# Kernel tuning notes

Measured on AMD Instinct MI355X. Metric: run time of the kernel, lower is better.

The kernel has to match this reference:

```python
import jax, jax.numpy as jnp
import numpy as np

DIM = 1024
FF = 4096
BATCH = 4
SEQ = 2048
EPS = 1e-5


def setup_inputs() -> dict:
    key = jax.random.key(0)
    ks = jax.random.split(key, 8)
    x = jax.random.normal(ks[0], (BATCH, SEQ, DIM), dtype=jnp.float32)
    # phazor init: exp(2j*pi*arange(dim)/dim) * |randn(dim)|
    ang = 2.0 * np.pi * jnp.arange(DIM, dtype=jnp.float32) / DIM
    mag = jnp.abs(jax.random.normal(ks[1], (DIM,), dtype=jnp.float32))
    phazor_re = mag * jnp.cos(ang)
    phazor_im = mag * jnp.sin(ang)
    last_re = jax.random.normal(ks[2], (DIM,), dtype=jnp.float32)
    last_im = jax.random.normal(ks[3], (DIM,), dtype=jnp.float32)
    w1 = jax.random.normal(ks[4], (FF, DIM), dtype=jnp.float32) * DIM ** -0.5
    b1 = jnp.zeros((FF,), dtype=jnp.float32)
    w2 = jax.random.normal(ks[5], (DIM, FF), dtype=jnp.float32) * FF ** -0.5
    b2 = jnp.zeros((DIM,), dtype=jnp.float32)
    return {
        'x': x,
        'ln1_w': jnp.ones((DIM,), jnp.float32), 'ln1_b': jnp.zeros((DIM,), jnp.float32),
        'ln2_w': jnp.ones((DIM,), jnp.float32), 'ln2_b': jnp.zeros((DIM,), jnp.float32),
        'sc_lin': jnp.ones((DIM,), jnp.float32),
        'phazor_re': phazor_re, 'phazor_im': phazor_im,
        'last_re': last_re, 'last_im': last_im,
        'w1': w1, 'b1': b1, 'w2': w2, 'b2': b2,
    }


def _layer_norm(x, w, b):
    mu = jnp.mean(x, axis=-1, keepdims=True)
    var = jnp.mean(jnp.square(x - mu), axis=-1, keepdims=True)
    return (x - mu) * jax.lax.rsqrt(var + EPS) * w + b


def _sconv(x, phazor_re, phazor_im, last_re, last_im):
    B, L, D = x.shape
    dtype = x.dtype
    xc = x.astype(jnp.complex64)
    p_raw = phazor_re + 1j * phazor_im
    # tanh(|p|) * exp(i*angle(p))
    p = (jnp.tanh(jnp.abs(p_raw)) * jnp.exp(1j * jnp.angle(p_raw))).astype(jnp.complex64)
    t = jnp.arange(L)[:, None]
    prog = jnp.power(p[None, :], t)            # [L, D] complex
    filt_fft = jnp.fft.fft(prog, n=2 * L, axis=0)   # [2L, D]
    x_fft = jnp.fft.fft(xc, n=2 * L, axis=1)        # [B, 2L, D]
    conv = jnp.fft.ifft(filt_fft[None] * x_fft, axis=1)[:, :L]  # [B, L, D]
    last = (last_re + 1j * last_im)[None, None, :]  # [1,1,D] broadcast over batch
    conv_with_past = conv + last * prog[None] * p[None, None]
    return conv_with_past.real.astype(dtype)


def reference(x, ln1_w, ln1_b, ln2_w, ln2_b, sc_lin,
              phazor_re, phazor_im, last_re, last_im,
              w1, b1, w2, b2):
    # SConv branch
    x_res = x
    h = _layer_norm(x, ln1_w, ln1_b)
    h = jax.nn.silu(h)
    h = _sconv(h, phazor_re, phazor_im, last_re, last_im)
    h = h * sc_lin
    x = h + x_res
    # FFN branch
    x_res = x
    h = _layer_norm(x, ln2_w, ln2_b)
    h = jax.nn.silu(jnp.einsum('bld,fd->blf', h, w1) + b1)
    h = jnp.einsum('blf,df->bld', h, w2) + b2
    return h + x_res
```

## Files before the change

kernel.cpp:

```cpp
#include <hip/hip_runtime.h>
#include <cmath>


#define DIMD 1024
#define FFD  4096
#define BATCH 4
#define SEQL 2048
#define MROWS (BATCH*SEQL)
#define EPSF 1e-5f
#define CHUNKS 32
#define CLEN (SEQL/CHUNKS)

typedef __attribute__((ext_vector_type(8))) _Float16 half8;
typedef __attribute__((ext_vector_type(4))) _Float16 half4;
typedef __attribute__((ext_vector_type(4))) float    floatx4;

#define H_OFF    0u
#define E_OFF    33554432u
#define SIN_OFF  34603008u
#define H2_OFF   35651584u
#define W1H_OFF  52428800u
#define W2H_OFF  60817408u
#define Y1_OFF   69206016u

__device__ __forceinline__ void load_lds16(const _Float16* g, _Float16* l) {
    __builtin_amdgcn_global_load_lds(
        (const __attribute__((address_space(1))) unsigned int*)g,
        (__attribute__((address_space(3))) unsigned int*)l,
        16, 0, 0);
}

__global__ __launch_bounds__(256)
void cast_f32_f16(const float* __restrict__ src, _Float16* __restrict__ dst) {
    int i = (blockIdx.x * 256 + threadIdx.x) * 4;
    float4 v = *(const float4*)(src + i);
    half4 o;
    o.x = (_Float16)v.x; o.y = (_Float16)v.y; o.z = (_Float16)v.z; o.w = (_Float16)v.w;
    *(half4*)(dst + i) = o;
}

__global__ __launch_bounds__(256)
void ln_kernel(const float* __restrict__ x, const float* __restrict__ w,
               const float* __restrict__ b, float* __restrict__ of,
               _Float16* __restrict__ oh, int mode) {
    const size_t row = blockIdx.x;
    const int tid = threadIdx.x;
    float4 v = *(const float4*)(x + row * DIMD + tid * 4);
    float s = (v.x + v.y) + (v.z + v.w);
    float q = (v.x * v.x + v.y * v.y) + (v.z * v.z + v.w * v.w);
    #pragma unroll
    for (int off = 32; off; off >>= 1) {
        s += __shfl_down(s, off, 64);
        q += __shfl_down(q, off, 64);
    }
    __shared__ float red[8];
    if (!(tid & 63)) { red[tid >> 6] = s; red[4 + (tid >> 6)] = q; }
    __syncthreads();
    s = (red[0] + red[1]) + (red[2] + red[3]);
    q = (red[4] + red[5]) + (red[6] + red[7]);
    const float mu = s * (1.f / DIMD);
    const float rs = rsqrtf(q * (1.f / DIMD) - mu * mu + EPSF);
    float4 wv = *(const float4*)(w + tid * 4);
    float4 bv = *(const float4*)(b + tid * 4);
    float o0 = (v.x - mu) * rs * wv.x + bv.x;
    float o1 = (v.y - mu) * rs * wv.y + bv.y;
    float o2 = (v.z - mu) * rs * wv.z + bv.z;
    float o3 = (v.w - mu) * rs * wv.w + bv.w;
    if (mode == 1) {
        o0 = o0 / (1.f + __expf(-o0));
        o1 = o1 / (1.f + __expf(-o1));
        o2 = o2 / (1.f + __expf(-o2));
        o3 = o3 / (1.f + __expf(-o3));
        float4 ov = {o0, o1, o2, o3};
        *(float4*)(of + row * DIMD + tid * 4) = ov;
    } else {
        half4 hv;
        hv.x = (_Float16)o0; hv.y = (_Float16)o1;
        hv.z = (_Float16)o2; hv.w = (_Float16)o3;
        *(half4*)(oh + row * DIMD + tid * 4) = hv;
    }
}

__device__ __forceinline__ void get_p(const float* pre, const float* pim, int d,
                                      float& pr, float& pi) {
    float re = pre[d], im = pim[d];
    float r = sqrtf(re * re + im * im);
    float t = tanhf(r) / fmaxf(r, 1e-30f);
    pr = re * t; pi = im * t;
}

__global__ __launch_bounds__(256)
void scan_partial(const float* __restrict__ h, const float* __restrict__ pre,
                  const float* __restrict__ pim, float2* __restrict__ e) {
    const int d = blockIdx.x * 256 + threadIdx.x;
    const int c = blockIdx.y;
    const int bb = blockIdx.z;
    float pr, pi; get_p(pre, pim, d, pr, pi);
    float sr = 0.f, si = 0.f;
    const float* hp = h + ((size_t)bb * SEQL + (size_t)c * CLEN) * DIMD + d;
    #pragma unroll 4
    for (int j = 0; j < CLEN; ++j) {
        float hv = hp[(size_t)j * DIMD];
        float nr = pr * sr - pi * si + hv;
        float ni = pr * si + pi * sr;
        sr = nr; si = ni;
    }
    e[((size_t)bb * CHUNKS + c) * DIMD + d] = make_float2(sr, si);
}

__global__ __launch_bounds__(256)
void scan_combine(const float2* __restrict__ e, const float* __restrict__ pre,
                  const float* __restrict__ pim, const float* __restrict__ lre,
                  const float* __restrict__ lim, float2* __restrict__ sv) {
    const int d = blockIdx.x * 256 + threadIdx.x;
    const int bb = blockIdx.y;
    float pr, pi; get_p(pre, pim, d, pr, pi);
    float qr = pr, qi = pi;
    #pragma unroll
    for (int s = 0; s < 6; ++s) {
        float nr = qr * qr - qi * qi;
        float ni = 2.f * qr * qi;
        qr = nr; qi = ni;
    }
    float sr = lre[d], si = lim[d];
    for (int c = 0; c < CHUNKS; ++c) {
        sv[((size_t)bb * CHUNKS + c) * DIMD + d] = make_float2(sr, si);
        float2 ec = e[((size_t)bb * CHUNKS + c) * DIMD + d];
        float nr = qr * sr - qi * si + ec.x;
        float ni = qr * si + qi * sr + ec.y;
        sr = nr; si = ni;
    }
}

__global__ __launch_bounds__(256)
void scan_final(const float* __restrict__ h, const float* __restrict__ x,
                const float* __restrict__ pre, const float* __restrict__ pim,
                const float* __restrict__ sc, const float2* __restrict__ sv,
                float* __restrict__ x2) {
    const int d = blockIdx.x * 256 + threadIdx.x;
    const int c = blockIdx.y;
    const int bb = blockIdx.z;
    float pr, pi; get_p(pre, pim, d, pr, pi);
    float2 s0 = sv[((size_t)bb * CHUNKS + c) * DIMD + d];
    float sr = s0.x, si = s0.y;
    const float scd = sc[d];
    const size_t base = ((size_t)bb * SEQL + (size_t)c * CLEN) * DIMD + d;
    #pragma unroll 4
    for (int j = 0; j < CLEN; ++j) {
        float hv = h[base + (size_t)j * DIMD];
        float nr = pr * sr - pi * si + hv;
        float ni = pr * si + pi * sr;
        sr = nr; si = ni;
        x2[base + (size_t)j * DIMD] = x[base + (size_t)j * DIMD] + scd * sr;
    }
}

#define BM 128
#define BN 128
#define BK 64

__global__ __launch_bounds__(256)
void gemm_bt(const _Float16* __restrict__ A, const _Float16* __restrict__ W,
             const float* __restrict__ bias, _Float16* __restrict__ out_h,
             const float* resid, float* out_f, int N, int K, int epi) {
    __shared__ _Float16 As[BM * BK];
    __shared__ _Float16 Bs[BN * BK];
    const int tid  = threadIdx.x;
    const int lane = tid & 63;
    const int wave = tid >> 6;
    const int wm = (wave >> 1) * 64;
    const int wn = (wave & 1) * 64;
    const size_t m0 = (size_t)blockIdx.y * BM;
    const size_t n0 = (size_t)blockIdx.x * BN;
    const int fr = lane & 15;
    const int quad = lane >> 4;

    const int srow = wave * 32 + (lane >> 3);
    const int ccp  = ((lane & 7) ^ (lane >> 3)) * 8;
    const _Float16* ag = A + (m0 + srow) * (size_t)K + ccp;
    const _Float16* wg = W + (n0 + srow) * (size_t)K + ccp;
    _Float16* asl = &As[(wave * 32) * BK];
    _Float16* bsl = &Bs[(wave * 32) * BK];

    floatx4 acc[4][4] = {};

    for (int k0 = 0; k0 < K; k0 += BK) {
        #pragma unroll
        for (int t = 0; t < 4; ++t) {
            load_lds16(ag + k0 + (size_t)(t * 8) * K, asl + t * 8 * BK);
            load_lds16(wg + k0 + (size_t)(t * 8) * K, bsl + t * 8 * BK);
        }
        __syncthreads();
        #pragma unroll
        for (int kk = 0; kk < BK; kk += 32) {
            half8 af[4], bf[4];
            #pragma unroll
            for (int i = 0; i < 4; ++i) {
                const int slot = (((kk >> 3) + quad) ^ (fr & 7)) * 8;
                af[i] = *(const half8*)(&As[(wm + i * 16 + fr) * BK + slot]);
                bf[i] = *(const half8*)(&Bs[(wn + i * 16 + fr) * BK + slot]);
            }
            #pragma unroll
            for (int i = 0; i < 4; ++i)
                #pragma unroll
                for (int j = 0; j < 4; ++j)
                    acc[i][j] = __builtin_amdgcn_mfma_f32_16x16x32_f16(
                        af[i], bf[j], acc[i][j], 0, 0, 0);
        }
        __syncthreads();
    }

    #pragma unroll
    for (int i = 0; i < 4; ++i) {
        #pragma unroll
        for (int j = 0; j < 4; ++j) {
            #pragma unroll
            for (int r = 0; r < 4; ++r) {
                const size_t gm = m0 + wm + i * 16 + quad * 4 + r;
                const size_t gn = n0 + wn + j * 16 + fr;
                float v = acc[i][j][r] + bias[gn];
                if (epi == 1) {
                    float sl = v / (1.f + __expf(-v));
                    out_h[gm * N + gn] = (_Float16)sl;
                } else {
                    out_f[gm * N + gn] = v + resid[gm * N + gn];
                }
            }
        }
    }
}

extern "C" void kernel_launch(void* const* d_in, const int* in_sizes, int n_in,
                              void* d_out, int out_size, void* d_ws, size_t ws_size,
                              hipStream_t stream) {
    const float* x    = (const float*)d_in[0];
    const float* ln1w = (const float*)d_in[1];
    const float* ln1b = (const float*)d_in[2];
    const float* ln2w = (const float*)d_in[3];
    const float* ln2b = (const float*)d_in[4];
    const float* sc   = (const float*)d_in[5];
    const float* pre  = (const float*)d_in[6];
    const float* pim  = (const float*)d_in[7];
    const float* lre  = (const float*)d_in[8];
    const float* lim  = (const float*)d_in[9];
    const float* w1   = (const float*)d_in[10];
    const float* b1   = (const float*)d_in[11];
    const float* w2   = (const float*)d_in[12];
    const float* b2   = (const float*)d_in[13];

    char* ws = (char*)d_ws;
    float*      h   = (float*)(ws + H_OFF);
    float2*     e   = (float2*)(ws + E_OFF);
    float2*     sv  = (float2*)(ws + SIN_OFF);
    _Float16*   h2  = (_Float16*)(ws + H2_OFF);
    _Float16*   w1h = (_Float16*)(ws + W1H_OFF);
    _Float16*   w2h = (_Float16*)(ws + W2H_OFF);
    _Float16*   y1  = (_Float16*)(ws + Y1_OFF);
    float*      x2  = (float*)d_out;
    float*      outp = (float*)d_out;

    cast_f32_f16<<<dim3(FFD * DIMD / 1024), 256, 0, stream>>>(w1, w1h);
    cast_f32_f16<<<dim3(FFD * DIMD / 1024), 256, 0, stream>>>(w2, w2h);
    ln_kernel<<<dim3(MROWS), 256, 0, stream>>>(x, ln1w, ln1b, h, nullptr, 1);
    scan_partial<<<dim3(DIMD / 256, CHUNKS, BATCH), 256, 0, stream>>>(h, pre, pim, e);
    scan_combine<<<dim3(DIMD / 256, BATCH), 256, 0, stream>>>(e, pre, pim, lre, lim, sv);
    scan_final<<<dim3(DIMD / 256, CHUNKS, BATCH), 256, 0, stream>>>(h, x, pre, pim, sc, sv, x2);
    ln_kernel<<<dim3(MROWS), 256, 0, stream>>>(x2, ln2w, ln2b, nullptr, h2, 2);
    gemm_bt<<<dim3(FFD / BN, MROWS / BM), 256, 0, stream>>>(
        h2, w1h, b1, y1, nullptr, nullptr, FFD, DIMD, 1);
    gemm_bt<<<dim3(DIMD / BN, MROWS / BM), 256, 0, stream>>>(
        y1, w2h, b2, nullptr, x2, outp, DIMD, FFD, 2);
}
```

Before: 382.4 us.

## Fuse layernorms and SiLU into chunked scan passes, merge weight casts

Each scan pass now owns one (chunk, batch) row block and recomputes LN1 and SiLU on the fly, so the fp32 intermediate h buffer disappears. The second pass also computes LN2 and writes the fp16 GEMM input directly, which removes both standalone layernorm kernels and their global round trips. Chunk count is raised to 128 to keep enough blocks, and the two weight casts are merged into one launch. In exchange, LN1 is recomputed in both passes, each row step needs block-wide barriers, and only 512 blocks run the sequential loops.

```diff
diff --git a/kernel.cpp b/kernel.cpp
--- a/kernel.cpp
+++ b/kernel.cpp
@@ -8,20 +8,19 @@
 #define SEQL 2048
 #define MROWS (BATCH*SEQL)
 #define EPSF 1e-5f
-#define CHUNKS 32
+#define CHUNKS 128
 #define CLEN (SEQL/CHUNKS)
 
 typedef __attribute__((ext_vector_type(8))) _Float16 half8;
 typedef __attribute__((ext_vector_type(4))) _Float16 half4;
 typedef __attribute__((ext_vector_type(4))) float    floatx4;
 
-#define H_OFF    0u
-#define E_OFF    33554432u
-#define SIN_OFF  34603008u
-#define H2_OFF   35651584u
-#define W1H_OFF  52428800u
-#define W2H_OFF  60817408u
-#define Y1_OFF   69206016u
+#define E_OFF    0u
+#define SV_OFF   4194304u
+#define H2_OFF   8388608u
+#define W1H_OFF  25165824u
+#define W2H_OFF  33554432u
+#define Y1_OFF   41943040u
 
 __device__ __forceinline__ void load_lds16(const _Float16* g, _Float16* l) {
     __builtin_amdgcn_global_load_lds(
@@ -30,54 +29,11 @@
         16, 0, 0);
 }
 
-__global__ __launch_bounds__(256)
-void cast_f32_f16(const float* __restrict__ src, _Float16* __restrict__ dst) {
-    int i = (blockIdx.x * 256 + threadIdx.x) * 4;
-    float4 v = *(const float4*)(src + i);
-    half4 o;
-    o.x = (_Float16)v.x; o.y = (_Float16)v.y; o.z = (_Float16)v.z; o.w = (_Float16)v.w;
-    *(half4*)(dst + i) = o;
-}
-
-__global__ __launch_bounds__(256)
-void ln_kernel(const float* __restrict__ x, const float* __restrict__ w,
-               const float* __restrict__ b, float* __restrict__ of,
-               _Float16* __restrict__ oh, int mode) {
-    const size_t row = blockIdx.x;
-    const int tid = threadIdx.x;
-    float4 v = *(const float4*)(x + row * DIMD + tid * 4);
-    float s = (v.x + v.y) + (v.z + v.w);
-    float q = (v.x * v.x + v.y * v.y) + (v.z * v.z + v.w * v.w);
+__device__ __forceinline__ void wave_reduce2(float& s, float& q) {
     #pragma unroll
     for (int off = 32; off; off >>= 1) {
         s += __shfl_down(s, off, 64);
         q += __shfl_down(q, off, 64);
-    }
-    __shared__ float red[8];
-    if (!(tid & 63)) { red[tid >> 6] = s; red[4 + (tid >> 6)] = q; }
-    __syncthreads();
-    s = (red[0] + red[1]) + (red[2] + red[3]);
-    q = (red[4] + red[5]) + (red[6] + red[7]);
-    const float mu = s * (1.f / DIMD);
-    const float rs = rsqrtf(q * (1.f / DIMD) - mu * mu + EPSF);
-    float4 wv = *(const float4*)(w + tid * 4);
-    float4 bv = *(const float4*)(b + tid * 4);
-    float o0 = (v.x - mu) * rs * wv.x + bv.x;
-    float o1 = (v.y - mu) * rs * wv.y + bv.y;
-    float o2 = (v.z - mu) * rs * wv.z + bv.z;
-    float o3 = (v.w - mu) * rs * wv.w + bv.w;
-    if (mode == 1) {
-        o0 = o0 / (1.f + __expf(-o0));
-        o1 = o1 / (1.f + __expf(-o1));
-        o2 = o2 / (1.f + __expf(-o2));
-        o3 = o3 / (1.f + __expf(-o3));
-        float4 ov = {o0, o1, o2, o3};
-        *(float4*)(of + row * DIMD + tid * 4) = ov;
-    } else {
-        half4 hv;
-        hv.x = (_Float16)o0; hv.y = (_Float16)o1;
-        hv.z = (_Float16)o2; hv.w = (_Float16)o3;
-        *(half4*)(oh + row * DIMD + tid * 4) = hv;
     }
 }
 
@@ -90,22 +46,62 @@
 }
 
 __global__ __launch_bounds__(256)
-void scan_partial(const float* __restrict__ h, const float* __restrict__ pre,
-                  const float* __restrict__ pim, float2* __restrict__ e) {
-    const int d = blockIdx.x * 256 + threadIdx.x;
-    const int c = blockIdx.y;
-    const int bb = blockIdx.z;
-    float pr, pi; get_p(pre, pim, d, pr, pi);
-    float sr = 0.f, si = 0.f;
-    const float* hp = h + ((size_t)bb * SEQL + (size_t)c * CLEN) * DIMD + d;
-    #pragma unroll 4
+void cast2_f32_f16(const float* __restrict__ w1, const float* __restrict__ w2,
+                   _Float16* __restrict__ o1, _Float16* __restrict__ o2) {
+    int i = (blockIdx.x * 256 + threadIdx.x) * 4;
+    const float* src = w1;
+    _Float16* dst = o1;
+    if (i >= FFD * DIMD) { i -= FFD * DIMD; src = w2; dst = o2; }
+    float4 v = *(const float4*)(src + i);
+    half4 o;
+    o.x = (_Float16)v.x; o.y = (_Float16)v.y; o.z = (_Float16)v.z; o.w = (_Float16)v.w;
+    *(half4*)(dst + i) = o;
+}
+
+__global__ __launch_bounds__(256)
+void scan_phase1(const float* __restrict__ x, const float* __restrict__ lw,
+                 const float* __restrict__ lb, const float* __restrict__ pre,
+                 const float* __restrict__ pim, float2* __restrict__ e) {
+    const int tid = threadIdx.x;
+    const int d0 = tid * 4;
+    const int c = blockIdx.x, bb = blockIdx.y;
+    const int lane = tid & 63, wave = tid >> 6;
+    __shared__ float2 red[2][4];
+
+    float pr[4], pi[4], sr[4] = {}, si[4] = {};
+    #pragma unroll
+    for (int q = 0; q < 4; ++q) get_p(pre, pim, d0 + q, pr[q], pi[q]);
+    const float4 wv = *(const float4*)(lw + d0);
+    const float4 bv = *(const float4*)(lb + d0);
+    const size_t rowbase = ((size_t)bb * SEQL + (size_t)c * CLEN) * DIMD;
+
     for (int j = 0; j < CLEN; ++j) {
-        float hv = hp[(size_t)j * DIMD];
-        float nr = pr * sr - pi * si + hv;
-        float ni = pr * si + pi * sr;
-        sr = nr; si = ni;
-    }
-    e[((size_t)bb * CHUNKS + c) * DIMD + d] = make_float2(sr, si);
+        float4 v = *(const float4*)(x + rowbase + (size_t)j * DIMD + d0);
+        float s = (v.x + v.y) + (v.z + v.w);
+        float q2 = (v.x * v.x + v.y * v.y) + (v.z * v.z + v.w * v.w);
+        wave_reduce2(s, q2);
+        if (lane == 0) red[j & 1][wave] = make_float2(s, q2);
+        __syncthreads();
+        float2 r0 = red[j & 1][0], r1 = red[j & 1][1];
+        float2 r2 = red[j & 1][2], r3 = red[j & 1][3];
+        s = (r0.x + r1.x) + (r2.x + r3.x);
+        q2 = (r0.y + r1.y) + (r2.y + r3.y);
+        const float mu = s * (1.f / DIMD);
+        const float rs = rsqrtf(q2 * (1.f / DIMD) - mu * mu + EPSF);
+        float o[4] = {
+            (v.x - mu) * rs * wv.x + bv.x, (v.y - mu) * rs * wv.y + bv.y,
+            (v.z - mu) * rs * wv.z + bv.z, (v.w - mu) * rs * wv.w + bv.w };
+        #pragma unroll
+        for (int q = 0; q < 4; ++q) {
+            float hv = o[q] / (1.f + __expf(-o[q]));
+            float nr = pr[q] * sr[q] - pi[q] * si[q] + hv;
+            float ni = pr[q] * si[q] + pi[q] * sr[q];
+            sr[q] = nr; si[q] = ni;
+        }
+    }
+    float2* ep = e + ((size_t)bb * CHUNKS + c) * DIMD + d0;
+    #pragma unroll
+    for (int q = 0; q < 4; ++q) ep[q] = make_float2(sr[q], si[q]);
 }
 
 __global__ __launch_bounds__(256)
@@ -117,15 +113,17 @@
     float pr, pi; get_p(pre, pim, d, pr, pi);
     float qr = pr, qi = pi;
     #pragma unroll
-    for (int s = 0; s < 6; ++s) {
+    for (int s = 0; s < 4; ++s) {
         float nr = qr * qr - qi * qi;
         float ni = 2.f * qr * qi;
         qr = nr; qi = ni;
     }
     float sr = lre[d], si = lim[d];
+    #pragma unroll 4
     for (int c = 0; c < CHUNKS; ++c) {
-        sv[((size_t)bb * CHUNKS + c) * DIMD + d] = make_float2(sr, si);
-        float2 ec = e[((size_t)bb * CHUNKS + c) * DIMD + d];
+        const size_t idx = ((size_t)bb * CHUNKS + c) * DIMD + d;
+        sv[idx] = make_float2(sr, si);
+        float2 ec = e[idx];
         float nr = qr * sr - qi * si + ec.x;
         float ni = qr * si + qi * sr + ec.y;
         sr = nr; si = ni;
@@ -133,25 +131,83 @@
 }
 
 __global__ __launch_bounds__(256)
-void scan_final(const float* __restrict__ h, const float* __restrict__ x,
-                const float* __restrict__ pre, const float* __restrict__ pim,
-                const float* __restrict__ sc, const float2* __restrict__ sv,
-                float* __restrict__ x2) {
-    const int d = blockIdx.x * 256 + threadIdx.x;
-    const int c = blockIdx.y;
-    const int bb = blockIdx.z;
-    float pr, pi; get_p(pre, pim, d, pr, pi);
-    float2 s0 = sv[((size_t)bb * CHUNKS + c) * DIMD + d];
-    float sr = s0.x, si = s0.y;
-    const float scd = sc[d];
-    const size_t base = ((size_t)bb * SEQL + (size_t)c * CLEN) * DIMD + d;
-    #pragma unroll 4
+void scan_phase2(const float* __restrict__ x, const float* __restrict__ l1w,
+                 const float* __restrict__ l1b, const float* __restrict__ l2w,
+                 const float* __restrict__ l2b, const float* __restrict__ pre,
+                 const float* __restrict__ pim, const float* __restrict__ sc,
+                 const float2* __restrict__ sv, float* __restrict__ x2,
+                 _Float16* __restrict__ h2) {
+    const int tid = threadIdx.x;
+    const int d0 = tid * 4;
+    const int c = blockIdx.x, bb = blockIdx.y;
+    const int lane = tid & 63, wave = tid >> 6;
+    __shared__ float2 redA[2][4];
+    __shared__ float2 redB[2][4];
+
+    float pr[4], pi[4], sr[4], si[4];
+    #pragma unroll
+    for (int q = 0; q < 4; ++q) {
+        get_p(pre, pim, d0 + q, pr[q], pi[q]);
+        float2 s0 = sv[((size_t)bb * CHUNKS + c) * DIMD + d0 + q];
+        sr[q] = s0.x; si[q] = s0.y;
+    }
+    const float4 w1v = *(const float4*)(l1w + d0);
+    const float4 b1v = *(const float4*)(l1b + d0);
+    const float4 w2v = *(const float4*)(l2w + d0);
+    const float4 b2v = *(const float4*)(l2b + d0);
+    const float4 scv = *(const float4*)(sc + d0);
+    const size_t rowbase = ((size_t)bb * SEQL + (size_t)c * CLEN) * DIMD;
+
     for (int j = 0; j < CLEN; ++j) {
-        float hv = h[base + (size_t)j * DIMD];
-        float nr = pr * sr - pi * si + hv;
-        float ni = pr * si + pi * sr;
-        sr = nr; si = ni;
-        x2[base + (size_t)j * DIMD] = x[base + (size_t)j * DIMD] + scd * sr;
+        float4 v = *(const float4*)(x + rowbase + (size_t)j * DIMD + d0);
+        float s = (v.x + v.y) + (v.z + v.w);
+        float q2 = (v.x * v.x + v.y * v.y) + (v.z * v.z + v.w * v.w);
+        wave_reduce2(s, q2);
+        if (lane == 0) redA[j & 1][wave] = make_float2(s, q2);
+        __syncthreads();
+        {
+            float2 r0 = redA[j & 1][0], r1 = redA[j & 1][1];
+            float2 r2 = redA[j & 1][2], r3 = redA[j & 1][3];
+            s = (r0.x + r1.x) + (r2.x + r3.x);
+            q2 = (r0.y + r1.y) + (r2.y + r3.y);
+        }
+        const float mu = s * (1.f / DIMD);
+        const float rs = rsqrtf(q2 * (1.f / DIMD) - mu * mu + EPSF);
+        float o[4] = {
+            (v.x - mu) * rs * w1v.x + b1v.x, (v.y - mu) * rs * w1v.y + b1v.y,
+            (v.z - mu) * rs * w1v.z + b1v.z, (v.w - mu) * rs * w1v.w + b1v.w };
+        #pragma unroll
+        for (int q = 0; q < 4; ++q) {
+            float hv = o[q] / (1.f + __expf(-o[q]));
+            float nr = pr[q] * sr[q] - pi[q] * si[q] + hv;
+            float ni = pr[q] * si[q] + pi[q] * sr[q];
+            sr[q] = nr; si[q] = ni;
+        }
+        float4 xv;
+        xv.x = v.x + scv.x * sr[0];
+        xv.y = v.y + scv.y * sr[1];
+        xv.z = v.z + scv.z * sr[2];
+        xv.w = v.w + scv.w * sr[3];
+        *(float4*)(x2 + rowbase + (size_t)j * DIMD + d0) = xv;
+        float s2 = (xv.x + xv.y) + (xv.z + xv.w);
+        float q3 = (xv.x * xv.x + xv.y * xv.y) + (xv.z * xv.z + xv.w * xv.w);
+        wave_reduce2(s2, q3);
+        if (lane == 0) redB[j & 1][wave] = make_float2(s2, q3);
+        __syncthreads();
+        {
+            float2 r0 = redB[j & 1][0], r1 = redB[j & 1][1];
+            float2 r2 = redB[j & 1][2], r3 = redB[j & 1][3];
+            s2 = (r0.x + r1.x) + (r2.x + r3.x);
+            q3 = (r0.y + r1.y) + (r2.y + r3.y);
+        }
+        const float mu2 = s2 * (1.f / DIMD);
+        const float rs2 = rsqrtf(q3 * (1.f / DIMD) - mu2 * mu2 + EPSF);
+        half4 hh;
+        hh.x = (_Float16)((xv.x - mu2) * rs2 * w2v.x + b2v.x);
+        hh.y = (_Float16)((xv.y - mu2) * rs2 * w2v.y + b2v.y);
+        hh.z = (_Float16)((xv.z - mu2) * rs2 * w2v.z + b2v.z);
+        hh.w = (_Float16)((xv.w - mu2) * rs2 * w2v.w + b2v.w);
+        *(half4*)(h2 + rowbase + (size_t)j * DIMD + d0) = hh;
     }
 }
 
@@ -249,9 +305,8 @@
     const float* b2   = (const float*)d_in[13];
 
     char* ws = (char*)d_ws;
-    float*      h   = (float*)(ws + H_OFF);
     float2*     e   = (float2*)(ws + E_OFF);
-    float2*     sv  = (float2*)(ws + SIN_OFF);
+    float2*     sv  = (float2*)(ws + SV_OFF);
     _Float16*   h2  = (_Float16*)(ws + H2_OFF);
     _Float16*   w1h = (_Float16*)(ws + W1H_OFF);
     _Float16*   w2h = (_Float16*)(ws + W2H_OFF);
@@ -259,13 +314,11 @@
     float*      x2  = (float*)d_out;
     float*      outp = (float*)d_out;
 
-    cast_f32_f16<<<dim3(FFD * DIMD / 1024), 256, 0, stream>>>(w1, w1h);
-    cast_f32_f16<<<dim3(FFD * DIMD / 1024), 256, 0, stream>>>(w2, w2h);
-    ln_kernel<<<dim3(MROWS), 256, 0, stream>>>(x, ln1w, ln1b, h, nullptr, 1);
-    scan_partial<<<dim3(DIMD / 256, CHUNKS, BATCH), 256, 0, stream>>>(h, pre, pim, e);
+    cast2_f32_f16<<<dim3(2 * FFD * DIMD / 1024), 256, 0, stream>>>(w1, w2, w1h, w2h);
+    scan_phase1<<<dim3(CHUNKS, BATCH), 256, 0, stream>>>(x, ln1w, ln1b, pre, pim, e);
     scan_combine<<<dim3(DIMD / 256, BATCH), 256, 0, stream>>>(e, pre, pim, lre, lim, sv);
-    scan_final<<<dim3(DIMD / 256, CHUNKS, BATCH), 256, 0, stream>>>(h, x, pre, pim, sc, sv, x2);
-    ln_kernel<<<dim3(MROWS), 256, 0, stream>>>(x2, ln2w, ln2b, nullptr, h2, 2);
+    scan_phase2<<<dim3(CHUNKS, BATCH), 256, 0, stream>>>(
+        x, ln1w, ln1b, ln2w, ln2b, pre, pim, sc, sv, x2, h2);
     gemm_bt<<<dim3(FFD / BN, MROWS / BM), 256, 0, stream>>>(
         h2, w1h, b1, y1, nullptr, nullptr, FFD, DIMD, 1);
     gemm_bt<<<dim3(DIMD / BN, MROWS / BM), 256, 0, stream>>>(
```

After: 395.7 us. 3.5% more time.
